# Kernel optimization log

Measured on AMD Instinct MI355X. Metric: run time of the kernel, lower is better.

## Reference

```python
import jax, jax.numpy as jnp
import numpy as np

B, S, I, O = 64, 512, 256, 256


def setup_inputs() -> dict:
    key = jax.random.key(0)
    ks = jax.random.split(key, 7)
    s_i = 1.0 / np.sqrt(I)
    s_o = 1.0 / np.sqrt(O)
    return {
        "x": jax.random.normal(ks[0], (B, S, I), dtype=jnp.float32),
        "h0": jax.random.normal(ks[1], (B, O), dtype=jnp.float32) * 0.1,
        "c0": jax.random.normal(ks[2], (B, O), dtype=jnp.float32) * 0.1,
        # gate order: [f, i, g, o]; Linear convention y = x @ W.T + b
        "Wh": jax.random.normal(ks[3], (4, O, O), dtype=jnp.float32) * s_o,
        "bh": jax.random.normal(ks[4], (4, O), dtype=jnp.float32) * s_o,
        "Wx": jax.random.normal(ks[5], (4, O, I), dtype=jnp.float32) * s_i,
        "bx": jax.random.normal(ks[6], (4, O), dtype=jnp.float32) * s_i,
    }


def reference(x, h0, c0, Wh, bh, Wx, bx):
    # Precompute all input-side gate projections in one big GEMM: [S, B, 4, O]
    xg = jnp.einsum('bsi,goi->sbgo', x, Wx) + bx + bh  # fold both biases here

    def step(carry, xt):
        h, c = carry
        g = jnp.einsum('bo,gpo->bgp', h, Wh) + xt  # [B, 4, O]
        f = jax.nn.sigmoid(g[:, 0])
        i = jax.nn.sigmoid(g[:, 1])
        gt = jnp.tanh(g[:, 2])
        o = jax.nn.sigmoid(g[:, 3])
        c = c * f + i * gt
        h = o * jnp.tanh(c)
        return (h, c), h

    (hT, cT), hs = jax.lax.scan(step, (h0, c0), xg)
    h_seq = jnp.transpose(hs, (1, 0, 2))  # [B, S, O]
    return h_seq, hT, cT
```

## Files before the change

### kernel.cpp

```cpp
#include <hip/hip_runtime.h>


#define SS 512

typedef _Float16 v8h __attribute__((ext_vector_type(8)));
typedef float vf4 __attribute__((ext_vector_type(4)));

__device__ __forceinline__ float sigm(float x) { return 1.f / (1.f + __expf(-x)); }
__device__ __forceinline__ float tanh_f(float x) {
  float e = __expf(-2.f * fabsf(x));
  float r = (1.f - e) / (1.f + e);
  return copysignf(r, x);
}

__global__ __launch_bounds__(256) void xg_gemm(
    const float* __restrict__ X, const float* __restrict__ W,
    const float* __restrict__ bx, const float* __restrict__ bh,
    float* __restrict__ out)
{
  __shared__ float As[64][68];
  __shared__ float Bs[64][68];
  const int bm = blockIdx.x >> 4;
  const int bn = blockIdx.x & 15;
  const int tid = threadIdx.x;
  const int tn = tid & 15, tm = tid >> 4;
  const int row0 = bm * 64, col0 = bn * 64;
  float acc[4][4] = {};

  for (int k0 = 0; k0 < 256; k0 += 64) {
#pragma unroll
    for (int i = 0; i < 4; i++) {
      const int m = (tid >> 4) + i * 16;
      const int k = (tid & 15) * 4;
      float4 av = *(const float4*)&X[(size_t)(row0 + m) * 256 + k0 + k];
      *(float4*)&As[m][k] = av;
      float4 wv = *(const float4*)&W[(size_t)(col0 + m) * 256 + k0 + k];
      Bs[k + 0][m] = wv.x; Bs[k + 1][m] = wv.y;
      Bs[k + 2][m] = wv.z; Bs[k + 3][m] = wv.w;
    }
    __syncthreads();
#pragma unroll 8
    for (int kk = 0; kk < 64; kk++) {
      const float a0 = As[tm * 4 + 0][kk];
      const float a1 = As[tm * 4 + 1][kk];
      const float a2 = As[tm * 4 + 2][kk];
      const float a3 = As[tm * 4 + 3][kk];
      const float4 bv = *(const float4*)&Bs[kk][tn * 4];
      acc[0][0] = fmaf(a0, bv.x, acc[0][0]); acc[0][1] = fmaf(a0, bv.y, acc[0][1]);
      acc[0][2] = fmaf(a0, bv.z, acc[0][2]); acc[0][3] = fmaf(a0, bv.w, acc[0][3]);
      acc[1][0] = fmaf(a1, bv.x, acc[1][0]); acc[1][1] = fmaf(a1, bv.y, acc[1][1]);
      acc[1][2] = fmaf(a1, bv.z, acc[1][2]); acc[1][3] = fmaf(a1, bv.w, acc[1][3]);
      acc[2][0] = fmaf(a2, bv.x, acc[2][0]); acc[2][1] = fmaf(a2, bv.y, acc[2][1]);
      acc[2][2] = fmaf(a2, bv.z, acc[2][2]); acc[2][3] = fmaf(a2, bv.w, acc[2][3]);
      acc[3][0] = fmaf(a3, bv.x, acc[3][0]); acc[3][1] = fmaf(a3, bv.y, acc[3][1]);
      acc[3][2] = fmaf(a3, bv.z, acc[3][2]); acc[3][3] = fmaf(a3, bv.w, acc[3][3]);
    }
    __syncthreads();
  }

  float bias[4];
#pragma unroll
  for (int j = 0; j < 4; j++) {
    const int col = col0 + tn * 4 + j;
    bias[j] = bx[col] + bh[col];
  }
#pragma unroll
  for (int i = 0; i < 4; i++) {
    float4 o4;
    o4.x = acc[i][0] + bias[0]; o4.y = acc[i][1] + bias[1];
    o4.z = acc[i][2] + bias[2]; o4.w = acc[i][3] + bias[3];
    *(float4*)&out[(size_t)(row0 + tm * 4 + i) * 1024 + col0 + tn * 4] = o4;
  }
}

__global__ __launch_bounds__(512) void lstm_scan5(
    const float* __restrict__ xg,
    const float* __restrict__ Wh,
    const float* __restrict__ h0,
    const float* __restrict__ c0,
    float* __restrict__ out)
{
  __shared__ __align__(16) _Float16 wtail[8 * 8 * 2 * 64 * 8];
  __shared__ __align__(16) _Float16 hbuf[2][256];
  __shared__ __align__(16) float ylds[4][256];

  const int tid  = threadIdx.x;
  const int b    = blockIdx.x;
  const int w    = tid >> 6;
  const int lane = tid & 63;
  const int q    = lane >> 4;
  const int l15  = lane & 15;

  v8h A[8][6];
#pragma unroll
  for (int j = 0; j < 8; ++j) {
    const int g = j >> 1, i = j & 1;
    const float* rp = Wh + (size_t)(g * 256 + w * 32 + i * 16 + l15) * 256 + q * 8;
#pragma unroll
    for (int kf = 0; kf < 6; ++kf) {
      float4 lo = *(const float4*)(rp + kf * 32);
      float4 hi = *(const float4*)(rp + kf * 32 + 4);
      v8h a;
      a[0] = (_Float16)lo.x; a[1] = (_Float16)lo.y;
      a[2] = (_Float16)lo.z; a[3] = (_Float16)lo.w;
      a[4] = (_Float16)hi.x; a[5] = (_Float16)hi.y;
      a[6] = (_Float16)hi.z; a[7] = (_Float16)hi.w;
      A[j][kf] = a;
    }
#pragma unroll
    for (int kfi = 0; kfi < 2; ++kfi) {
      float4 lo = *(const float4*)(rp + 192 + kfi * 32);
      float4 hi = *(const float4*)(rp + 192 + kfi * 32 + 4);
      _Float16* dst = &wtail[((((w * 8 + j) * 2) + kfi) * 64 + lane) * 8];
      dst[0] = (_Float16)lo.x; dst[1] = (_Float16)lo.y;
      dst[2] = (_Float16)lo.z; dst[3] = (_Float16)lo.w;
      dst[4] = (_Float16)hi.x; dst[5] = (_Float16)hi.y;
      dst[6] = (_Float16)hi.z; dst[7] = (_Float16)hi.w;
    }
  }

  if (tid < 256) hbuf[0][tid] = (_Float16)h0[(size_t)b * 256 + tid];
  float c = (tid < 256) ? c0[(size_t)b * 256 + tid] : 0.f;
  __syncthreads();

  const float* xb = xg + (size_t)b * SS * 1024;
  float* hs = out + (size_t)b * SS * 256;
  float hprev = 0.f;

  for (int t = 0; t < SS; ++t) {
    const int par = t & 1;

    float xc0 = 0.f, xc1 = 0.f, xc2 = 0.f, xc3 = 0.f;
    if (tid < 256) {
      if (t > 0) hs[(size_t)(t - 1) * 256 + tid] = hprev;
      const float* xp = xb + (size_t)t * 1024 + tid;
      xc0 = xp[0]; xc1 = xp[256]; xc2 = xp[512]; xc3 = xp[768];
    }

    vf4 D[8];
#pragma unroll
    for (int j = 0; j < 8; ++j) { vf4 z = {0.f, 0.f, 0.f, 0.f}; D[j] = z; }

#pragma unroll
    for (int kf = 0; kf < 6; ++kf) {
      v8h Bf = *(const v8h*)&hbuf[par][kf * 32 + q * 8];
#pragma unroll
      for (int j = 0; j < 8; ++j)
        D[j] = __builtin_amdgcn_mfma_f32_16x16x32_f16(A[j][kf], Bf, D[j], 0, 0, 0);
    }
#pragma unroll
    for (int kfi = 0; kfi < 2; ++kfi) {
      v8h Bf = *(const v8h*)&hbuf[par][(6 + kfi) * 32 + q * 8];
#pragma unroll
      for (int j = 0; j < 8; ++j) {
        v8h wt = *(const v8h*)&wtail[((((w * 8 + j) * 2) + kfi) * 64 + lane) * 8];
        D[j] = __builtin_amdgcn_mfma_f32_16x16x32_f16(wt, Bf, D[j], 0, 0, 0);
      }
    }

    if (l15 == 0) {
#pragma unroll
      for (int j = 0; j < 8; ++j) {
        const int g = j >> 1, i = j & 1;
        *(vf4*)&ylds[g][w * 32 + i * 16 + q * 4] = D[j];
      }
    }
    __syncthreads();

    if (tid < 256) {
      const float y0 = ylds[0][tid] + xc0;
      const float y1 = ylds[1][tid] + xc1;
      const float y2 = ylds[2][tid] + xc2;
      const float y3 = ylds[3][tid] + xc3;
      const float fg = sigm(y0);
      const float ig = sigm(y1);
      const float gt = tanh_f(y2);
      const float og = sigm(y3);
      c = c * fg + ig * gt;
      const float h = og * tanh_f(c);
      hprev = h;
      hbuf[par ^ 1][tid] = (_Float16)h;
    }
    __syncthreads();
  }

  if (tid < 256) {
    hs[(size_t)(SS - 1) * 256 + tid] = hprev;
    out[8388608 + (size_t)b * 256 + tid] = hprev;
    out[8404992 + (size_t)b * 256 + tid] = c;
  }
}

extern "C" void kernel_launch(void* const* d_in, const int* in_sizes, int n_in,
                              void* d_out, int out_size, void* d_ws, size_t ws_size,
                              hipStream_t stream) {
  const float* x  = (const float*)d_in[0];
  const float* h0 = (const float*)d_in[1];
  const float* c0 = (const float*)d_in[2];
  const float* Wh = (const float*)d_in[3];
  const float* bh = (const float*)d_in[4];
  const float* Wx = (const float*)d_in[5];
  const float* bx = (const float*)d_in[6];
  float* out = (float*)d_out;

  float* xg = (float*)d_ws;

  xg_gemm<<<dim3(8192), dim3(256), 0, stream>>>(x, Wx, bx, bh, xg);
  lstm_scan5<<<dim3(64), dim3(512), 0, stream>>>(xg, Wh, h0, c0, out);
}
```

Baseline: 1.323 ms.

## Halve scan block to 4 waves, each computing 16 gate tiles

```diff
diff --git a/kernel.cpp b/kernel.cpp
--- a/kernel.cpp
+++ b/kernel.cpp
@@ -73,14 +73,14 @@
   }
 }
 
-__global__ __launch_bounds__(512) void lstm_scan5(
+__global__ __launch_bounds__(256, 1) void lstm_scan6(
     const float* __restrict__ xg,
     const float* __restrict__ Wh,
     const float* __restrict__ h0,
     const float* __restrict__ c0,
     float* __restrict__ out)
 {
-  __shared__ __align__(16) _Float16 wtail[8 * 8 * 2 * 64 * 8];
+  __shared__ __align__(16) _Float16 wtail[4][16][2][64][8];
   __shared__ __align__(16) _Float16 hbuf[2][256];
   __shared__ __align__(16) float ylds[4][256];
 
@@ -91,11 +91,11 @@
   const int q    = lane >> 4;
   const int l15  = lane & 15;
 
-  v8h A[8][6];
-#pragma unroll
-  for (int j = 0; j < 8; ++j) {
-    const int g = j >> 1, i = j & 1;
-    const float* rp = Wh + (size_t)(g * 256 + w * 32 + i * 16 + l15) * 256 + q * 8;
+  v8h A[16][6];
+#pragma unroll
+  for (int j = 0; j < 16; ++j) {
+    const int g = j >> 2, i = j & 3;
+    const float* rp = Wh + (size_t)(g * 256 + w * 64 + i * 16 + l15) * 256 + q * 8;
 #pragma unroll
     for (int kf = 0; kf < 6; ++kf) {
       float4 lo = *(const float4*)(rp + kf * 32);
@@ -111,7 +111,7 @@
     for (int kfi = 0; kfi < 2; ++kfi) {
       float4 lo = *(const float4*)(rp + 192 + kfi * 32);
       float4 hi = *(const float4*)(rp + 192 + kfi * 32 + 4);
-      _Float16* dst = &wtail[((((w * 8 + j) * 2) + kfi) * 64 + lane) * 8];
+      _Float16* dst = &wtail[w][j][kfi][lane][0];
       dst[0] = (_Float16)lo.x; dst[1] = (_Float16)lo.y;
       dst[2] = (_Float16)lo.z; dst[3] = (_Float16)lo.w;
       dst[4] = (_Float16)hi.x; dst[5] = (_Float16)hi.y;
@@ -119,8 +119,8 @@
     }
   }
 
-  if (tid < 256) hbuf[0][tid] = (_Float16)h0[(size_t)b * 256 + tid];
-  float c = (tid < 256) ? c0[(size_t)b * 256 + tid] : 0.f;
+  hbuf[0][tid] = (_Float16)h0[(size_t)b * 256 + tid];
+  float c = c0[(size_t)b * 256 + tid];
   __syncthreads();
 
   const float* xb = xg + (size_t)b * SS * 1024;
@@ -130,65 +130,60 @@
   for (int t = 0; t < SS; ++t) {
     const int par = t & 1;
 
-    float xc0 = 0.f, xc1 = 0.f, xc2 = 0.f, xc3 = 0.f;
-    if (tid < 256) {
-      if (t > 0) hs[(size_t)(t - 1) * 256 + tid] = hprev;
-      const float* xp = xb + (size_t)t * 1024 + tid;
-      xc0 = xp[0]; xc1 = xp[256]; xc2 = xp[512]; xc3 = xp[768];
-    }
-
-    vf4 D[8];
-#pragma unroll
-    for (int j = 0; j < 8; ++j) { vf4 z = {0.f, 0.f, 0.f, 0.f}; D[j] = z; }
-
-#pragma unroll
-    for (int kf = 0; kf < 6; ++kf) {
-      v8h Bf = *(const v8h*)&hbuf[par][kf * 32 + q * 8];
-#pragma unroll
-      for (int j = 0; j < 8; ++j)
-        D[j] = __builtin_amdgcn_mfma_f32_16x16x32_f16(A[j][kf], Bf, D[j], 0, 0, 0);
-    }
-#pragma unroll
-    for (int kfi = 0; kfi < 2; ++kfi) {
-      v8h Bf = *(const v8h*)&hbuf[par][(6 + kfi) * 32 + q * 8];
-#pragma unroll
-      for (int j = 0; j < 8; ++j) {
-        v8h wt = *(const v8h*)&wtail[((((w * 8 + j) * 2) + kfi) * 64 + lane) * 8];
-        D[j] = __builtin_amdgcn_mfma_f32_16x16x32_f16(wt, Bf, D[j], 0, 0, 0);
+    if (t > 0) hs[(size_t)(t - 1) * 256 + tid] = hprev;
+    const float* xp = xb + (size_t)t * 1024 + tid;
+    const float xc0 = xp[0], xc1 = xp[256], xc2 = xp[512], xc3 = xp[768];
+
+#pragma unroll
+    for (int pass = 0; pass < 2; ++pass) {
+      vf4 D[8];
+#pragma unroll
+      for (int jj = 0; jj < 8; ++jj) { vf4 z = {0.f, 0.f, 0.f, 0.f}; D[jj] = z; }
+#pragma unroll
+      for (int kf = 0; kf < 6; ++kf) {
+        v8h Bf = *(const v8h*)&hbuf[par][kf * 32 + q * 8];
+#pragma unroll
+        for (int jj = 0; jj < 8; ++jj)
+          D[jj] = __builtin_amdgcn_mfma_f32_16x16x32_f16(
+              A[pass * 8 + jj][kf], Bf, D[jj], 0, 0, 0);
       }
-    }
-
-    if (l15 == 0) {
-#pragma unroll
-      for (int j = 0; j < 8; ++j) {
-        const int g = j >> 1, i = j & 1;
-        *(vf4*)&ylds[g][w * 32 + i * 16 + q * 4] = D[j];
+#pragma unroll
+      for (int kfi = 0; kfi < 2; ++kfi) {
+        v8h Bf = *(const v8h*)&hbuf[par][(6 + kfi) * 32 + q * 8];
+#pragma unroll
+        for (int jj = 0; jj < 8; ++jj) {
+          v8h wt = *(const v8h*)&wtail[w][pass * 8 + jj][kfi][lane][0];
+          D[jj] = __builtin_amdgcn_mfma_f32_16x16x32_f16(wt, Bf, D[jj], 0, 0, 0);
+        }
       }
-    }
-    __syncthreads();
-
-    if (tid < 256) {
-      const float y0 = ylds[0][tid] + xc0;
-      const float y1 = ylds[1][tid] + xc1;
-      const float y2 = ylds[2][tid] + xc2;
-      const float y3 = ylds[3][tid] + xc3;
-      const float fg = sigm(y0);
-      const float ig = sigm(y1);
-      const float gt = tanh_f(y2);
-      const float og = sigm(y3);
-      c = c * fg + ig * gt;
-      const float h = og * tanh_f(c);
-      hprev = h;
-      hbuf[par ^ 1][tid] = (_Float16)h;
-    }
-    __syncthreads();
-  }
-
-  if (tid < 256) {
-    hs[(size_t)(SS - 1) * 256 + tid] = hprev;
-    out[8388608 + (size_t)b * 256 + tid] = hprev;
-    out[8404992 + (size_t)b * 256 + tid] = c;
-  }
+      if (l15 == 0) {
+#pragma unroll
+        for (int jj = 0; jj < 8; ++jj) {
+          const int j = pass * 8 + jj, g = j >> 2, i = j & 3;
+          *(vf4*)&ylds[g][w * 64 + i * 16 + q * 4] = D[jj];
+        }
+      }
+    }
+    __syncthreads();
+
+    const float y0 = ylds[0][tid] + xc0;
+    const float y1 = ylds[1][tid] + xc1;
+    const float y2 = ylds[2][tid] + xc2;
+    const float y3 = ylds[3][tid] + xc3;
+    const float fg = sigm(y0);
+    const float ig = sigm(y1);
+    const float gt = tanh_f(y2);
+    const float og = sigm(y3);
+    c = c * fg + ig * gt;
+    const float h = og * tanh_f(c);
+    hprev = h;
+    hbuf[par ^ 1][tid] = (_Float16)h;
+    __syncthreads();
+  }
+
+  hs[(size_t)(SS - 1) * 256 + tid] = hprev;
+  out[8388608 + (size_t)b * 256 + tid] = hprev;
+  out[8404992 + (size_t)b * 256 + tid] = c;
 }
 
 extern "C" void kernel_launch(void* const* d_in, const int* in_sizes, int n_in,
@@ -206,5 +201,5 @@
   float* xg = (float*)d_ws;
 
   xg_gemm<<<dim3(8192), dim3(256), 0, stream>>>(x, Wx, bx, bh, xg);
-  lstm_scan5<<<dim3(64), dim3(512), 0, stream>>>(xg, Wh, h0, c0, out);
-}
+  lstm_scan6<<<dim3(64), dim3(256), 0, stream>>>(xg, Wh, h0, c0, out);
+}
```

Result: slower. 1.648 ms (+24.6%).

## Compute LSTM gates in MFMA-owning lanes and drop one barrier per step

Applied to the files above, without the earlier changes.

```diff
diff --git a/kernel.cpp b/kernel.cpp
--- a/kernel.cpp
+++ b/kernel.cpp
@@ -4,6 +4,7 @@
 #define SS 512
 
 typedef _Float16 v8h __attribute__((ext_vector_type(8)));
+typedef _Float16 v4h __attribute__((ext_vector_type(4)));
 typedef float vf4 __attribute__((ext_vector_type(4)));
 
 __device__ __forceinline__ float sigm(float x) { return 1.f / (1.f + __expf(-x)); }
@@ -73,16 +74,16 @@
   }
 }
 
-__global__ __launch_bounds__(512) void lstm_scan5(
+__global__ __launch_bounds__(512) void lstm_scan7(
     const float* __restrict__ xg,
     const float* __restrict__ Wh,
     const float* __restrict__ h0,
     const float* __restrict__ c0,
     float* __restrict__ out)
 {
-  __shared__ __align__(16) _Float16 wtail[8 * 8 * 2 * 64 * 8];
+  __shared__ __align__(16) _Float16 wtail[8][8][2][64][8];
   __shared__ __align__(16) _Float16 hbuf[2][256];
-  __shared__ __align__(16) float ylds[4][256];
+  __shared__ __align__(16) float xld[2][1024];
 
   const int tid  = threadIdx.x;
   const int b    = blockIdx.x;
@@ -90,6 +91,8 @@
   const int lane = tid & 63;
   const int q    = lane >> 4;
   const int l15  = lane & 15;
+  const bool act = (l15 == 0);
+  const int pb   = w * 32 + q * 4;
 
   v8h A[8][6];
 #pragma unroll
@@ -111,7 +114,7 @@
     for (int kfi = 0; kfi < 2; ++kfi) {
       float4 lo = *(const float4*)(rp + 192 + kfi * 32);
       float4 hi = *(const float4*)(rp + 192 + kfi * 32 + 4);
-      _Float16* dst = &wtail[((((w * 8 + j) * 2) + kfi) * 64 + lane) * 8];
+      _Float16* dst = &wtail[w][j][kfi][lane][0];
       dst[0] = (_Float16)lo.x; dst[1] = (_Float16)lo.y;
       dst[2] = (_Float16)lo.z; dst[3] = (_Float16)lo.w;
       dst[4] = (_Float16)hi.x; dst[5] = (_Float16)hi.y;
@@ -120,74 +123,100 @@
   }
 
   if (tid < 256) hbuf[0][tid] = (_Float16)h0[(size_t)b * 256 + tid];
-  float c = (tid < 256) ? c0[(size_t)b * 256 + tid] : 0.f;
+  const float* xb = xg + (size_t)b * SS * 1024;
+  {
+    float2 v = *(const float2*)&xb[2 * tid];
+    *(float2*)&xld[0][2 * tid] = v;
+  }
+  float4 cs[2] = {{0, 0, 0, 0}, {0, 0, 0, 0}};
+  float4 hp[2] = {{0, 0, 0, 0}, {0, 0, 0, 0}};
+  if (act) {
+#pragma unroll
+    for (int i = 0; i < 2; ++i)
+      cs[i] = *(const float4*)&c0[(size_t)b * 256 + pb + i * 16];
+  }
   __syncthreads();
 
-  const float* xb = xg + (size_t)b * SS * 1024;
   float* hs = out + (size_t)b * SS * 256;
-  float hprev = 0.f;
 
   for (int t = 0; t < SS; ++t) {
-    const int par = t & 1;
-
-    float xc0 = 0.f, xc1 = 0.f, xc2 = 0.f, xc3 = 0.f;
-    if (tid < 256) {
-      if (t > 0) hs[(size_t)(t - 1) * 256 + tid] = hprev;
-      const float* xp = xb + (size_t)t * 1024 + tid;
-      xc0 = xp[0]; xc1 = xp[256]; xc2 = xp[512]; xc3 = xp[768];
-    }
-
-    vf4 D[8];
-#pragma unroll
-    for (int j = 0; j < 8; ++j) { vf4 z = {0.f, 0.f, 0.f, 0.f}; D[j] = z; }
-
-#pragma unroll
-    for (int kf = 0; kf < 6; ++kf) {
-      v8h Bf = *(const v8h*)&hbuf[par][kf * 32 + q * 8];
-#pragma unroll
-      for (int j = 0; j < 8; ++j)
-        D[j] = __builtin_amdgcn_mfma_f32_16x16x32_f16(A[j][kf], Bf, D[j], 0, 0, 0);
-    }
-#pragma unroll
-    for (int kfi = 0; kfi < 2; ++kfi) {
-      v8h Bf = *(const v8h*)&hbuf[par][(6 + kfi) * 32 + q * 8];
-#pragma unroll
-      for (int j = 0; j < 8; ++j) {
-        v8h wt = *(const v8h*)&wtail[((((w * 8 + j) * 2) + kfi) * 64 + lane) * 8];
-        D[j] = __builtin_amdgcn_mfma_f32_16x16x32_f16(wt, Bf, D[j], 0, 0, 0);
+    const int cb = t & 1, nb = cb ^ 1;
+
+    float2 xpre = {0.f, 0.f};
+    if (t + 1 < SS) xpre = *(const float2*)&xb[(size_t)(t + 1) * 1024 + 2 * tid];
+
+    if (t > 0 && act) {
+      *(float4*)&hs[(size_t)(t - 1) * 256 + pb] = hp[0];
+      *(float4*)&hs[(size_t)(t - 1) * 256 + pb + 16] = hp[1];
+    }
+
+#pragma unroll
+    for (int pass = 0; pass < 2; ++pass) {
+      vf4 D[4];
+#pragma unroll
+      for (int g = 0; g < 4; ++g) { vf4 z = {0.f, 0.f, 0.f, 0.f}; D[g] = z; }
+#pragma unroll
+      for (int kf = 0; kf < 6; ++kf) {
+        v8h Bf = *(const v8h*)&hbuf[cb][kf * 32 + q * 8];
+#pragma unroll
+        for (int g = 0; g < 4; ++g)
+          D[g] = __builtin_amdgcn_mfma_f32_16x16x32_f16(
+              A[g * 2 + pass][kf], Bf, D[g], 0, 0, 0);
       }
-    }
-
-    if (l15 == 0) {
-#pragma unroll
-      for (int j = 0; j < 8; ++j) {
-        const int g = j >> 1, i = j & 1;
-        *(vf4*)&ylds[g][w * 32 + i * 16 + q * 4] = D[j];
+#pragma unroll
+      for (int kfi = 0; kfi < 2; ++kfi) {
+        v8h Bf = *(const v8h*)&hbuf[cb][(6 + kfi) * 32 + q * 8];
+#pragma unroll
+        for (int g = 0; g < 4; ++g) {
+          v8h wt = *(const v8h*)&wtail[w][g * 2 + pass][kfi][lane][0];
+          D[g] = __builtin_amdgcn_mfma_f32_16x16x32_f16(wt, Bf, D[g], 0, 0, 0);
+        }
       }
-    }
+
+      if (act) {
+        const int P = pb + pass * 16;
+        float4 xf = *(const float4*)&xld[cb][0 * 256 + P];
+        float4 xi = *(const float4*)&xld[cb][1 * 256 + P];
+        float4 xgv = *(const float4*)&xld[cb][2 * 256 + P];
+        float4 xo = *(const float4*)&xld[cb][3 * 256 + P];
+        float hv[4];
+        float* cp = (float*)&cs[pass];
+        const float* xfp = (const float*)&xf;
+        const float* xip = (const float*)&xi;
+        const float* xgp = (const float*)&xgv;
+        const float* xop = (const float*)&xo;
+#pragma unroll
+        for (int r = 0; r < 4; ++r) {
+          const float fg = sigm(D[0][r] + xfp[r]);
+          const float ig = sigm(D[1][r] + xip[r]);
+          const float gt = tanh_f(D[2][r] + xgp[r]);
+          const float og = sigm(D[3][r] + xop[r]);
+          const float cn = cp[r] * fg + ig * gt;
+          cp[r] = cn;
+          hv[r] = og * tanh_f(cn);
+        }
+        float4* hpp = &hp[pass];
+        (*hpp).x = hv[0]; (*hpp).y = hv[1]; (*hpp).z = hv[2]; (*hpp).w = hv[3];
+        v4h h4;
+        h4[0] = (_Float16)hv[0]; h4[1] = (_Float16)hv[1];
+        h4[2] = (_Float16)hv[2]; h4[3] = (_Float16)hv[3];
+        *(v4h*)&hbuf[nb][P] = h4;
+      }
+    }
+
+    if (t + 1 < SS) *(float2*)&xld[nb][2 * tid] = xpre;
+
     __syncthreads();
-
-    if (tid < 256) {
-      const float y0 = ylds[0][tid] + xc0;
-      const float y1 = ylds[1][tid] + xc1;
-      const float y2 = ylds[2][tid] + xc2;
-      const float y3 = ylds[3][tid] + xc3;
-      const float fg = sigm(y0);
-      const float ig = sigm(y1);
-      const float gt = tanh_f(y2);
-      const float og = sigm(y3);
-      c = c * fg + ig * gt;
-      const float h = og * tanh_f(c);
-      hprev = h;
-      hbuf[par ^ 1][tid] = (_Float16)h;
-    }
-    __syncthreads();
-  }
-
-  if (tid < 256) {
-    hs[(size_t)(SS - 1) * 256 + tid] = hprev;
-    out[8388608 + (size_t)b * 256 + tid] = hprev;
-    out[8404992 + (size_t)b * 256 + tid] = c;
+  }
+
+  if (act) {
+    *(float4*)&hs[(size_t)(SS - 1) * 256 + pb] = hp[0];
+    *(float4*)&hs[(size_t)(SS - 1) * 256 + pb + 16] = hp[1];
+#pragma unroll
+    for (int i = 0; i < 2; ++i) {
+      *(float4*)&out[8388608 + (size_t)b * 256 + pb + i * 16] = hp[i];
+      *(float4*)&out[8404992 + (size_t)b * 256 + pb + i * 16] = cs[i];
+    }
   }
 }
 
@@ -206,5 +235,5 @@
   float* xg = (float*)d_ws;
 
   xg_gemm<<<dim3(8192), dim3(256), 0, stream>>>(x, Wx, bx, bh, xg);
-  lstm_scan5<<<dim3(64), dim3(512), 0, stream>>>(xg, Wh, h0, c0, out);
-}
+  lstm_scan7<<<dim3(64), dim3(512), 0, stream>>>(xg, Wh, h0, c0, out);
+}
```

New measurement: 2.889 ms. 2.18x slower.
